# Optimization experiments

Hardware: AMD Instinct MI355X
Metric: run time of the kernel (lower is better)

Reference implementation:

```python
import jax, jax.numpy as jnp
import numpy as np

B, L, D = 2, 2048, 512
H = 8
DH = D // H
MAX_DIST = 2048
DFC = 2048


def setup_inputs() -> dict:
    key = jax.random.key(0)
    ks = jax.random.split(key, 12)
    w = lambda k, shape: (jax.random.normal(k, shape, jnp.float32) * 0.02)
    x = jax.random.normal(ks[0], (B, L, D), jnp.float32)
    # additive causal mask: 0 on/below diagonal, -1e9 above
    mask = jnp.where(jnp.triu(jnp.ones((L, L), bool), 1), -1e9, 0.0).astype(jnp.float32)
    return {
        "x": x,
        "mask": mask,
        "wq": w(ks[1], (D, D)), "bq": jnp.zeros((D,), jnp.float32),
        "wk": w(ks[2], (D, D)), "bk": jnp.zeros((D,), jnp.float32),
        "wv": w(ks[3], (D, D)), "bv": jnp.zeros((D,), jnp.float32),
        "rel_emb": w(ks[4], (MAX_DIST, D)),
        "w1": w(ks[5], (D, DFC)), "b1": jnp.zeros((DFC,), jnp.float32),
        "w2": w(ks[6], (DFC, D)), "b2": jnp.zeros((D,), jnp.float32),
    }


def skew(q_e):
    # Huang et al. sec 3.4: pad one column on the left, reshape (L, L+1)->(L+1, L), drop first row
    b, h, l, _ = q_e.shape
    padded = jnp.pad(q_e, ((0, 0), (0, 0), (0, 0), (1, 0)))  # (B,H,L,L+1)
    return padded.reshape(b, h, l + 1, l)[:, :, 1:, :]        # (B,H,L,L)


def reference(x, mask, wq, bq, wk, bk, wv, bv, rel_emb, w1, b1, w2, b2):
    b, l, d = x.shape
    q = (x @ wq + bq).reshape(b, l, H, DH)
    k = (x @ wk + bk).reshape(b, l, H, DH)
    v = (x @ wv + bv).reshape(b, l, H, DH)
    # relative position embeddings for the last l positions
    e = rel_emb[rel_emb.shape[0] - l:].reshape(l, H, DH)       # (L,H,DH)
    q_e = jnp.einsum('blhd,mhd->bhlm', q, e)                   # QE^T
    s_rel = skew(q_e)
    qk = jnp.einsum('blhd,bmhd->bhlm', q, k)                   # QK^T
    logits = (qk + s_rel) / jnp.sqrt(jnp.float32(DH)) + mask
    a = jax.nn.softmax(logits, axis=-1)
    attn = jnp.einsum('bhlm,bmhd->blhd', a, v).reshape(b, l, d)
    h = jax.nn.relu(attn @ w1 + b1)  # dropout is identity in eval mode
    return h @ w2 + b2
```

## Files before the change

### kernel.cpp

```cpp
#include <hip/hip_runtime.h>
#include <cstdint>

#define B_   2
#define L_   2048
#define D_   512
#define H_   8
#define DH_  64
#define DFC_ 2048

typedef unsigned short ushort_t;
typedef __attribute__((ext_vector_type(8))) short bf16x8;
typedef __attribute__((ext_vector_type(4))) short bf16x4;
typedef __attribute__((ext_vector_type(4))) float f32x4;

#define MFMA32(A, Bv, C) __builtin_amdgcn_mfma_f32_16x16x32_bf16(A, Bv, C, 0, 0, 0)
#define MFMA16(A, Bv, C) __builtin_amdgcn_mfma_f32_16x16x16bf16_1k(A, Bv, C, 0, 0, 0)

__device__ __forceinline__ ushort_t f32_bf16(float f) {
  unsigned u = __float_as_uint(f);
  u += 0x7FFFu + ((u >> 16) & 1u);
  return (ushort_t)(u >> 16);
}
__device__ __forceinline__ float bf16_f32(ushort_t u) {
  return __uint_as_float(((unsigned)u) << 16);
}

__device__ __forceinline__ void gl_lds16(const ushort_t* g, ushort_t* l) {
  __builtin_amdgcn_global_load_lds(
      (const __attribute__((address_space(1))) void*)(const void*)g,
      (__attribute__((address_space(3))) void*)l, 16, 0, 0);
}

__global__ __launch_bounds__(256)
void pack_x_rel(const float* __restrict__ x, const float* __restrict__ rel,
                ushort_t* __restrict__ xb, ushort_t* __restrict__ relb) {
  const int bid = blockIdx.x;
  const float* in = (bid < 1024) ? x : rel;
  ushort_t* out = (bid < 1024) ? xb : relb;
  const int base = (bid < 1024) ? bid : (bid - 1024);
  int i = (base * 256 + threadIdx.x) * 8;
  float4 a = *(const float4*)(in + i);
  float4 b = *(const float4*)(in + i + 4);
  union { bf16x8 v; ushort_t s[8]; } u;
  u.s[0] = f32_bf16(a.x); u.s[1] = f32_bf16(a.y);
  u.s[2] = f32_bf16(a.z); u.s[3] = f32_bf16(a.w);
  u.s[4] = f32_bf16(b.x); u.s[5] = f32_bf16(b.y);
  u.s[6] = f32_bf16(b.z); u.s[7] = f32_bf16(b.w);
  *(bf16x8*)(out + i) = u.v;
}

__global__ __launch_bounds__(256)
void packT_all(const float* __restrict__ wq, const float* __restrict__ wk,
               const float* __restrict__ wv, const float* __restrict__ w1,
               const float* __restrict__ w2, ushort_t* __restrict__ wqkvT,
               ushort_t* __restrict__ w1T, ushort_t* __restrict__ w2T) {
  __shared__ float T[64 * 65];
  const int id = blockIdx.x;
  const float* in; ushort_t* out; int K, N, bx, by;
  if (id < 192) {
    int z = id >> 6, r = id & 63;
    in = (z == 0) ? wq : (z == 1) ? wk : wv;
    out = wqkvT + (size_t)z * 512 * 512;
    K = 512; N = 512; bx = r & 7; by = r >> 3;
  } else if (id < 448) {
    int r = id - 192;
    in = w1; out = w1T; K = 512; N = 2048; bx = r & 31; by = r >> 5;
  } else {
    int r = id - 448;
    in = w2; out = w2T; K = 2048; N = 512; bx = r & 7; by = r >> 3;
  }
  const int t = threadIdx.x;
  const int n0 = bx * 64, k0 = by * 64;
  {
    const int kr = t >> 2, c0 = (t & 3) * 16;
    const float* src = in + (size_t)(k0 + kr) * N + n0 + c0;
#pragma unroll
    for (int u = 0; u < 4; ++u) {
      float4 f = *(const float4*)(src + u * 4);
      T[kr * 65 + c0 + u * 4 + 0] = f.x;
      T[kr * 65 + c0 + u * 4 + 1] = f.y;
      T[kr * 65 + c0 + u * 4 + 2] = f.z;
      T[kr * 65 + c0 + u * 4 + 3] = f.w;
    }
  }
  __syncthreads();
  const int nr = t >> 2, kc0 = (t & 3) * 16;
  union { bf16x8 v; ushort_t s[8]; } o0, o1;
#pragma unroll
  for (int j = 0; j < 8; ++j) {
    o0.s[j] = f32_bf16(T[(kc0 + j) * 65 + nr]);
    o1.s[j] = f32_bf16(T[(kc0 + 8 + j) * 65 + nr]);
  }
  ushort_t* dst = out + (size_t)(n0 + nr) * K + k0 + kc0;
  *(bf16x8*)dst = o0.v;
  *(bf16x8*)(dst + 8) = o1.v;
}

template <int MODE>
__global__ __launch_bounds__(256, 2)
void gemm_mfma(const ushort_t* __restrict__ A, const ushort_t* __restrict__ Bt,
               const float* __restrict__ b0p, const float* __restrict__ b1p,
               const float* __restrict__ b2p,
               void* __restrict__ out0, void* __restrict__ out1, void* __restrict__ out2,
               int M, int N, int K, int ksplit) {
  __shared__ ushort_t As[128 * 32];
  __shared__ ushort_t Bs[128 * 32];

  const int t  = threadIdx.x;
  const int wv = t >> 6, ln = t & 63;
  const int l16 = ln & 15, lg = ln >> 4;
  const int n0 = blockIdx.x * 128, m0 = blockIdx.y * 128;
  const int mw = (wv >> 1) * 64, nw = (wv & 1) * 64;

  const int kchunk = K / ksplit;
  const int kbeg = blockIdx.z * kchunk, kend = kbeg + kchunk;

  f32x4 acc[4][4] = {};

  for (int k0 = kbeg; k0 < kend; k0 += 32) {
    __syncthreads();
#pragma unroll
    for (int i = 0; i < 2; ++i) {
      const int s = (i * 4 + wv) * 64 + ln;
      const int row = s >> 2, cs = s & 3;
      const int g = cs ^ ((row >> 1) & 3);
      gl_lds16(A + (size_t)(m0 + row) * K + k0 + g * 8, &As[(i * 4 + wv) * 512]);
      gl_lds16(Bt + (size_t)(n0 + row) * K + k0 + g * 8, &Bs[(i * 4 + wv) * 512]);
    }
    __syncthreads();

    bf16x8 af[4], bfr[4];
#pragma unroll
    for (int mi = 0; mi < 4; ++mi) {
      const int ri = mw + mi * 16 + l16;
      af[mi] = *(const bf16x8*)&As[ri * 32 + ((lg ^ ((ri >> 1) & 3)) * 8)];
    }
#pragma unroll
    for (int ni = 0; ni < 4; ++ni) {
      const int rj = nw + ni * 16 + l16;
      bfr[ni] = *(const bf16x8*)&Bs[rj * 32 + ((lg ^ ((rj >> 1) & 3)) * 8)];
    }
#pragma unroll
    for (int mi = 0; mi < 4; ++mi)
#pragma unroll
      for (int ni = 0; ni < 4; ++ni)
        acc[mi][ni] = MFMA32(af[mi], bfr[ni], acc[mi][ni]);
  }

  if (MODE == 0) {
    float* outp = (blockIdx.z == 0) ? (float*)out0 : (float*)out1;
#pragma unroll
    for (int mi = 0; mi < 4; ++mi)
#pragma unroll
      for (int reg = 0; reg < 4; ++reg) {
        const int m = m0 + mw + mi * 16 + lg * 4 + reg;
#pragma unroll
        for (int ni = 0; ni < 4; ++ni) {
          const int c = n0 + nw + ni * 16 + l16;
          outp[(size_t)m * N + c] = acc[mi][ni][reg];
        }
      }
  } else if (MODE == 1) {
    ushort_t* outp = (ushort_t*)out0;
#pragma unroll
    for (int mi = 0; mi < 4; ++mi)
#pragma unroll
      for (int reg = 0; reg < 4; ++reg) {
        const int m = m0 + mw + mi * 16 + lg * 4 + reg;
#pragma unroll
        for (int ni = 0; ni < 4; ++ni) {
          const int c = n0 + nw + ni * 16 + l16;
          float v = acc[mi][ni][reg] + b0p[c];
          outp[(size_t)m * N + c] = f32_bf16(fmaxf(v, 0.f));
        }
      }
  } else {
#pragma unroll
    for (int mi = 0; mi < 4; ++mi)
#pragma unroll
      for (int reg = 0; reg < 4; ++reg) {
        const int m = m0 + mw + mi * 16 + lg * 4 + reg;
        const int b = m >> 11, l = m & (L_ - 1);
#pragma unroll
        for (int ni = 0; ni < 4; ++ni) {
          const int c = n0 + nw + ni * 16 + l16;
          const int which = c >> 9, cc = c & 511;
          const int h = cc >> 6, dh = cc & 63;
          const float* bias = (which == 0) ? b0p : (which == 1) ? b1p : b2p;
          float v = acc[mi][ni][reg] + bias[cc];
          if (which == 0) {
            ((ushort_t*)out0)[(((size_t)b * H_ + h) * L_ + l) * DH_ + dh] =
                f32_bf16(v * 0.125f);
          } else if (which == 1) {
            ((ushort_t*)out1)[(((size_t)b * H_ + h) * L_ + l) * DH_ + dh] = f32_bf16(v);
          } else {
            ((ushort_t*)out2)[(((size_t)b * H_ + h) * DH_ + dh) * L_ + l] = f32_bf16(v);
          }
        }
      }
  }
}

__global__ __launch_bounds__(256)
void ffn2_add(float* __restrict__ out, const float* __restrict__ p1,
              const float* __restrict__ bias) {
  int i = (blockIdx.x * 256 + threadIdx.x) * 4;
  float4 a = *(const float4*)(out + i);
  float4 b = *(const float4*)(p1 + i);
  float4 bb = *(const float4*)(bias + (i & (D_ - 1)));
  a.x += b.x + bb.x; a.y += b.y + bb.y;
  a.z += b.z + bb.z; a.w += b.w + bb.w;
  *(float4*)(out + i) = a;
}

__global__ __launch_bounds__(256, 4)
void attn_mfma(const ushort_t* __restrict__ q16, const ushort_t* __restrict__ k16,
               const ushort_t* __restrict__ vT, const ushort_t* __restrict__ relb,
               float* __restrict__ Opart, float* __restrict__ Lpart) {
  __shared__ ushort_t Ks[64 * 64];
  __shared__ ushort_t Vs[64 * 64];
  __shared__ ushort_t Rc[64 * 136];

  const int t   = threadIdx.x;
  const int wv  = t >> 6;
  const int ln  = t & 63;
  const int l16 = ln & 15;
  const int lg  = ln >> 4;
  const int bh  = blockIdx.x;
  const int yy  = blockIdx.y;
  const int qb  = (yy < 16) ? yy : (47 - yy);
  const int z   = blockIdx.z;
  const int i0  = qb * 64;
  const int mid = (qb + 2) >> 1;
  const int kbeg = z ? mid : 0;
  const int kend = z ? (qb + 1) : mid;

  const ushort_t* qh = q16 + (size_t)bh * L_ * DH_;
  const ushort_t* kh = k16 + (size_t)bh * L_ * DH_;
  const ushort_t* vh = vT + (size_t)bh * DH_ * L_;
  const ushort_t* relh = relb + (bh & 7) * DH_;

  const int r64i = wv * 16 + l16;
  const int rrow = r64i * 136;

  bf16x8 qf0, qf1;
  {
    const ushort_t* qr = qh + (size_t)(i0 + r64i) * DH_ + lg * 8;
    qf0 = *(const bf16x8*)(qr);
    qf1 = *(const bf16x8*)(qr + 32);
  }

  const f32x4 zf = {0.f, 0.f, 0.f, 0.f};
  f32x4 Of[4] = {zf, zf, zf, zf};
  float lsum = 0.f;

  auto compute_R = [&](int mbase, int slotbase) {
#pragma unroll
    for (int cb = 0; cb < 4; ++cb) {
      const ushort_t* e = relh + (size_t)(mbase + cb * 16 + l16) * D_ + lg * 8;
      bf16x8 e0 = *(const bf16x8*)(e);
      bf16x8 e1 = *(const bf16x8*)(e + 32);
      f32x4 r = MFMA32(e0, qf0, zf);
      r = MFMA32(e1, qf1, r);
      ushort4 w;
      w.x = f32_bf16(r[0]); w.y = f32_bf16(r[1]);
      w.z = f32_bf16(r[2]); w.w = f32_bf16(r[3]);
      *(ushort4*)&Rc[rrow + slotbase + cb * 16 + lg * 4] = w;
      if (slotbase == 0 && cb == 0 && lg == 0)
        *(ushort4*)&Rc[rrow + 128] = w;
    }
  };

  if (kbeg < kend) {
    compute_R(L_ - 64 - i0 + kbeg * 64, (kbeg & 1) * 64);

    for (int kb = kbeg; kb < kend; ++kb) {
      const int j0 = kb * 64;
      __syncthreads();
#pragma unroll
      for (int i = 0; i < 2; ++i) {
        const int s = (i * 4 + wv) * 64 + ln;
        const int row = s >> 3, c = s & 7;
        const int g = c ^ (row & 7);
        gl_lds16(kh + (size_t)(j0 + row) * DH_ + g * 8, &Ks[(i * 4 + wv) * 512]);
        gl_lds16(vh + (size_t)row * L_ + j0 + g * 8, &Vs[(i * 4 + wv) * 512]);
      }
      if (kb < qb)
        compute_R(L_ - 64 - i0 + (kb + 1) * 64, ((kb + 1) & 1) * 64);
      __syncthreads();

      f32x4 sf[4];
#pragma unroll
      for (int cb = 0; cb < 4; ++cb) {
        const int j = cb * 16 + l16;
        const int sw = j & 7;
        bf16x8 k0 = *(const bf16x8*)&Ks[j * 64 + ((lg ^ sw) * 8)];
        bf16x8 k1 = *(const bf16x8*)&Ks[j * 64 + (((lg + 4) ^ sw) * 8)];
        f32x4 s = MFMA32(k0, qf0, zf);
        sf[cb] = MFMA32(k1, qf1, s);
      }

      const bool diag = (kb == qb);
      bf16x4 pa[4];
#pragma unroll
      for (int cb = 0; cb < 4; ++cb) {
        const int jj0 = cb * 16 + lg * 4;
        const int base = (j0 + jj0 + 63 - r64i) & 127;
        union { bf16x4 v; ushort_t s[4]; } pk;
#pragma unroll
        for (int reg = 0; reg < 4; ++reg) {
          float x = sf[cb][reg] + bf16_f32(Rc[rrow + base + reg]);
          if (diag && (jj0 + reg) > r64i) x = -1e30f;
          float p = __expf(x);
          lsum += p;
          pk.s[reg] = f32_bf16(p);
        }
        pa[cb] = pk.v;
      }

#pragma unroll
      for (int cb2 = 0; cb2 < 4; ++cb2) {
        const int dh = cb2 * 16 + l16;
        const int sw = dh & 7;
        const ushort_t* vrow = &Vs[dh * 64];
#pragma unroll
        for (int cb = 0; cb < 4; ++cb) {
          const int cc = cb * 2 + (lg >> 1);
          bf16x4 vf = *(const bf16x4*)&vrow[((cc ^ sw) * 8) + (lg & 1) * 4];
          Of[cb2] = MFMA16(vf, pa[cb], Of[cb2]);
        }
      }
    }
  }

  float tot = lsum;
  tot += __shfl_xor(tot, 16);
  tot += __shfl_xor(tot, 32);
  if (lg == 0)
    Lpart[((size_t)(z * 16 + bh)) * L_ + i0 + r64i] = tot;
  float* orow = Opart + (((size_t)(z * 16 + bh)) * L_ + i0 + r64i) * DH_;
#pragma unroll
  for (int cb2 = 0; cb2 < 4; ++cb2)
    *(f32x4*)&orow[cb2 * 16 + lg * 4] = Of[cb2];
}

__global__ __launch_bounds__(256)
void attn_combine(const float* __restrict__ Opart, const float* __restrict__ Lpart,
                  ushort_t* __restrict__ attnb) {
  const int g = blockIdx.x * 256 + threadIdx.x;
  const int dh4 = g & 15, i = (g >> 4) & (L_ - 1), bh = g >> 15;
  const size_t o0 = (((size_t)bh * L_ + i) * DH_) + dh4 * 4;
  const size_t zstride = (size_t)16 * L_ * DH_;
  float4 a = *(const float4*)(Opart + o0);
  float4 b = *(const float4*)(Opart + o0 + zstride);
  const float l = Lpart[(size_t)bh * L_ + i] + Lpart[(size_t)(16 + bh) * L_ + i];
  const float inv = 1.f / l;
  ushort4 o;
  o.x = f32_bf16((a.x + b.x) * inv);
  o.y = f32_bf16((a.y + b.y) * inv);
  o.z = f32_bf16((a.z + b.z) * inv);
  o.w = f32_bf16((a.w + b.w) * inv);
  const int bb = bh >> 3, h = bh & 7;
  *(ushort4*)(attnb + ((size_t)(bb * L_ + i)) * D_ + h * DH_ + dh4 * 4) = o;
}

extern "C" void kernel_launch(void* const* d_in, const int* in_sizes, int n_in,
                              void* d_out, int out_size, void* d_ws, size_t ws_size,
                              hipStream_t stream) {
  const float* x   = (const float*)d_in[0];
  const float* wq  = (const float*)d_in[2];
  const float* bq  = (const float*)d_in[3];
  const float* wk  = (const float*)d_in[4];
  const float* bk  = (const float*)d_in[5];
  const float* wv  = (const float*)d_in[6];
  const float* bv  = (const float*)d_in[7];
  const float* rel = (const float*)d_in[8];
  const float* w1  = (const float*)d_in[9];
  const float* b1  = (const float*)d_in[10];
  const float* w2  = (const float*)d_in[11];
  const float* b2  = (const float*)d_in[12];

  char* wsb = (char*)d_ws;
  const size_t MB = 1u << 20;
  ushort_t* xb     = (ushort_t*)(wsb + 0 * MB);
  ushort_t* attnb  = (ushort_t*)(wsb + 0 * MB);
  ushort_t* wqkvT  = (ushort_t*)(wsb + 4 * MB);
  ushort_t* w1T    = (ushort_t*)(wsb + 6 * MB);
  ushort_t* w2T    = (ushort_t*)(wsb + 8 * MB);
  ushort_t* relb   = (ushort_t*)(wsb + 10 * MB);
  ushort_t* q16    = (ushort_t*)(wsb + 12 * MB);
  ushort_t* k16    = (ushort_t*)(wsb + 16 * MB);
  ushort_t* vTb    = (ushort_t*)(wsb + 20 * MB);
  float*    Opart  = (float*)(wsb + 24 * MB);
  float*    Lpart  = (float*)(wsb + 40 * MB);
  ushort_t* hidb   = (ushort_t*)(wsb + 24 * MB);
  float*    p1     = (float*)(wsb + 12 * MB);
  float*    out    = (float*)d_out;

  dim3 blk(256);
  pack_x_rel<<<dim3(1536), blk, 0, stream>>>(x, rel, xb, relb);
  packT_all<<<dim3(704), blk, 0, stream>>>(wq, wk, wv, w1, w2, wqkvT, w1T, w2T);
  gemm_mfma<2><<<dim3(12, 32), blk, 0, stream>>>(
      xb, wqkvT, bq, bk, bv, q16, k16, vTb, B_ * L_, 1536, D_, 1);
  attn_mfma<<<dim3(16, 32, 2), blk, 0, stream>>>(q16, k16, vTb, relb, Opart, Lpart);
  attn_combine<<<dim3(2048), blk, 0, stream>>>(Opart, Lpart, attnb);
  gemm_mfma<1><<<dim3(16, 32), blk, 0, stream>>>(
      attnb, w1T, b1, nullptr, nullptr, hidb, nullptr, nullptr,
      B_ * L_, DFC_, D_, 1);
  gemm_mfma<0><<<dim3(4, 32, 2), blk, 0, stream>>>(
      hidb, w2T, nullptr, nullptr, nullptr, out, p1, nullptr,
      B_ * L_, D_, DFC_, 2);
  ffn2_add<<<dim3(2048), blk, 0, stream>>>(out, p1, b2);
}
```

Baseline: 232.9 us.

## Double-buffer LDS tiles in GEMM and attention, merge packing kernels

The GEMM and attention kernels now keep two LDS buffers for their A/B and K/V tiles. The next tile's global-to-LDS load is issued before computing on the current tile, and each loop iteration drops one barrier. This is meant to hide global load latency behind MFMA work. The cost is doubled LDS use, and the attention kernel's launch bound is lowered from 4 to 3 blocks per CU to fit it. The two input/weight packing kernels are also merged into one launch to save launch overhead.

```diff
diff --git a/kernel.cpp b/kernel.cpp
--- a/kernel.cpp
+++ b/kernel.cpp
@@ -32,30 +32,32 @@
 }
 
 __global__ __launch_bounds__(256)
-void pack_x_rel(const float* __restrict__ x, const float* __restrict__ rel,
-                ushort_t* __restrict__ xb, ushort_t* __restrict__ relb) {
+void pack_all(const float* __restrict__ x, const float* __restrict__ rel,
+              const float* __restrict__ wq, const float* __restrict__ wk,
+              const float* __restrict__ wv, const float* __restrict__ w1,
+              const float* __restrict__ w2,
+              ushort_t* __restrict__ xb, ushort_t* __restrict__ relb,
+              ushort_t* __restrict__ wqkvT, ushort_t* __restrict__ w1T,
+              ushort_t* __restrict__ w2T) {
+  __shared__ float T[64 * 65];
   const int bid = blockIdx.x;
-  const float* in = (bid < 1024) ? x : rel;
-  ushort_t* out = (bid < 1024) ? xb : relb;
-  const int base = (bid < 1024) ? bid : (bid - 1024);
-  int i = (base * 256 + threadIdx.x) * 8;
-  float4 a = *(const float4*)(in + i);
-  float4 b = *(const float4*)(in + i + 4);
-  union { bf16x8 v; ushort_t s[8]; } u;
-  u.s[0] = f32_bf16(a.x); u.s[1] = f32_bf16(a.y);
-  u.s[2] = f32_bf16(a.z); u.s[3] = f32_bf16(a.w);
-  u.s[4] = f32_bf16(b.x); u.s[5] = f32_bf16(b.y);
-  u.s[6] = f32_bf16(b.z); u.s[7] = f32_bf16(b.w);
-  *(bf16x8*)(out + i) = u.v;
-}
-
-__global__ __launch_bounds__(256)
-void packT_all(const float* __restrict__ wq, const float* __restrict__ wk,
-               const float* __restrict__ wv, const float* __restrict__ w1,
-               const float* __restrict__ w2, ushort_t* __restrict__ wqkvT,
-               ushort_t* __restrict__ w1T, ushort_t* __restrict__ w2T) {
-  __shared__ float T[64 * 65];
-  const int id = blockIdx.x;
+  const int t = threadIdx.x;
+  if (bid < 1536) {
+    const float* in = (bid < 1024) ? x : rel;
+    ushort_t* out = (bid < 1024) ? xb : relb;
+    const int base = (bid < 1024) ? bid : (bid - 1024);
+    int i = (base * 256 + t) * 8;
+    float4 a = *(const float4*)(in + i);
+    float4 b = *(const float4*)(in + i + 4);
+    union { bf16x8 v; ushort_t s[8]; } u;
+    u.s[0] = f32_bf16(a.x); u.s[1] = f32_bf16(a.y);
+    u.s[2] = f32_bf16(a.z); u.s[3] = f32_bf16(a.w);
+    u.s[4] = f32_bf16(b.x); u.s[5] = f32_bf16(b.y);
+    u.s[6] = f32_bf16(b.z); u.s[7] = f32_bf16(b.w);
+    *(bf16x8*)(out + i) = u.v;
+    return;
+  }
+  const int id = bid - 1536;
   const float* in; ushort_t* out; int K, N, bx, by;
   if (id < 192) {
     int z = id >> 6, r = id & 63;
@@ -69,7 +71,6 @@
     int r = id - 448;
     in = w2; out = w2T; K = 2048; N = 512; bx = r & 7; by = r >> 3;
   }
-  const int t = threadIdx.x;
   const int n0 = bx * 64, k0 = by * 64;
   {
     const int kr = t >> 2, c0 = (t & 3) * 16;
@@ -103,8 +104,8 @@
                const float* __restrict__ b2p,
                void* __restrict__ out0, void* __restrict__ out1, void* __restrict__ out2,
                int M, int N, int K, int ksplit) {
-  __shared__ ushort_t As[128 * 32];
-  __shared__ ushort_t Bs[128 * 32];
+  __shared__ ushort_t As[2][128 * 32];
+  __shared__ ushort_t Bs[2][128 * 32];
 
   const int t  = threadIdx.x;
   const int wv = t >> 6, ln = t & 63;
@@ -117,34 +118,40 @@
 
   f32x4 acc[4][4] = {};
 
-  for (int k0 = kbeg; k0 < kend; k0 += 32) {
-    __syncthreads();
+  auto stage = [&](int k0, int b) {
 #pragma unroll
     for (int i = 0; i < 2; ++i) {
       const int s = (i * 4 + wv) * 64 + ln;
       const int row = s >> 2, cs = s & 3;
       const int g = cs ^ ((row >> 1) & 3);
-      gl_lds16(A + (size_t)(m0 + row) * K + k0 + g * 8, &As[(i * 4 + wv) * 512]);
-      gl_lds16(Bt + (size_t)(n0 + row) * K + k0 + g * 8, &Bs[(i * 4 + wv) * 512]);
-    }
+      gl_lds16(A + (size_t)(m0 + row) * K + k0 + g * 8, &As[b][(i * 4 + wv) * 512]);
+      gl_lds16(Bt + (size_t)(n0 + row) * K + k0 + g * 8, &Bs[b][(i * 4 + wv) * 512]);
+    }
+  };
+
+  stage(kbeg, 0);
+  int buf = 0;
+  for (int k0 = kbeg; k0 < kend; k0 += 32) {
     __syncthreads();
+    if (k0 + 32 < kend) stage(k0 + 32, buf ^ 1);
 
     bf16x8 af[4], bfr[4];
 #pragma unroll
     for (int mi = 0; mi < 4; ++mi) {
       const int ri = mw + mi * 16 + l16;
-      af[mi] = *(const bf16x8*)&As[ri * 32 + ((lg ^ ((ri >> 1) & 3)) * 8)];
+      af[mi] = *(const bf16x8*)&As[buf][ri * 32 + ((lg ^ ((ri >> 1) & 3)) * 8)];
     }
 #pragma unroll
     for (int ni = 0; ni < 4; ++ni) {
       const int rj = nw + ni * 16 + l16;
-      bfr[ni] = *(const bf16x8*)&Bs[rj * 32 + ((lg ^ ((rj >> 1) & 3)) * 8)];
+      bfr[ni] = *(const bf16x8*)&Bs[buf][rj * 32 + ((lg ^ ((rj >> 1) & 3)) * 8)];
     }
 #pragma unroll
     for (int mi = 0; mi < 4; ++mi)
 #pragma unroll
       for (int ni = 0; ni < 4; ++ni)
         acc[mi][ni] = MFMA32(af[mi], bfr[ni], acc[mi][ni]);
+    buf ^= 1;
   }
 
   if (MODE == 0) {
@@ -213,12 +220,12 @@
   *(float4*)(out + i) = a;
 }
 
-__global__ __launch_bounds__(256, 4)
+__global__ __launch_bounds__(256, 3)
 void attn_mfma(const ushort_t* __restrict__ q16, const ushort_t* __restrict__ k16,
                const ushort_t* __restrict__ vT, const ushort_t* __restrict__ relb,
                float* __restrict__ Opart, float* __restrict__ Lpart) {
-  __shared__ ushort_t Ks[64 * 64];
-  __shared__ ushort_t Vs[64 * 64];
+  __shared__ ushort_t Ks[2][64 * 64];
+  __shared__ ushort_t Vs[2][64 * 64];
   __shared__ ushort_t Rc[64 * 136];
 
   const int t   = threadIdx.x;
@@ -254,6 +261,17 @@
   f32x4 Of[4] = {zf, zf, zf, zf};
   float lsum = 0.f;
 
+  auto stageKV = [&](int j0, int b) {
+#pragma unroll
+    for (int i = 0; i < 2; ++i) {
+      const int s = (i * 4 + wv) * 64 + ln;
+      const int row = s >> 3, c = s & 7;
+      const int g = c ^ (row & 7);
+      gl_lds16(kh + (size_t)(j0 + row) * DH_ + g * 8, &Ks[b][(i * 4 + wv) * 512]);
+      gl_lds16(vh + (size_t)row * L_ + j0 + g * 8, &Vs[b][(i * 4 + wv) * 512]);
+    }
+  };
+
   auto compute_R = [&](int mbase, int slotbase) {
 #pragma unroll
     for (int cb = 0; cb < 4; ++cb) {
@@ -272,30 +290,24 @@
   };
 
   if (kbeg < kend) {
+    stageKV(kbeg * 64, kbeg & 1);
     compute_R(L_ - 64 - i0 + kbeg * 64, (kbeg & 1) * 64);
 
     for (int kb = kbeg; kb < kend; ++kb) {
       const int j0 = kb * 64;
+      const int buf = kb & 1;
       __syncthreads();
-#pragma unroll
-      for (int i = 0; i < 2; ++i) {
-        const int s = (i * 4 + wv) * 64 + ln;
-        const int row = s >> 3, c = s & 7;
-        const int g = c ^ (row & 7);
-        gl_lds16(kh + (size_t)(j0 + row) * DH_ + g * 8, &Ks[(i * 4 + wv) * 512]);
-        gl_lds16(vh + (size_t)row * L_ + j0 + g * 8, &Vs[(i * 4 + wv) * 512]);
-      }
+      if (kb + 1 < kend) stageKV(j0 + 64, buf ^ 1);
       if (kb < qb)
         compute_R(L_ - 64 - i0 + (kb + 1) * 64, ((kb + 1) & 1) * 64);
-      __syncthreads();
 
       f32x4 sf[4];
 #pragma unroll
       for (int cb = 0; cb < 4; ++cb) {
         const int j = cb * 16 + l16;
         const int sw = j & 7;
-        bf16x8 k0 = *(const bf16x8*)&Ks[j * 64 + ((lg ^ sw) * 8)];
-        bf16x8 k1 = *(const bf16x8*)&Ks[j * 64 + (((lg + 4) ^ sw) * 8)];
+        bf16x8 k0 = *(const bf16x8*)&Ks[buf][j * 64 + ((lg ^ sw) * 8)];
+        bf16x8 k1 = *(const bf16x8*)&Ks[buf][j * 64 + (((lg + 4) ^ sw) * 8)];
         f32x4 s = MFMA32(k0, qf0, zf);
         sf[cb] = MFMA32(k1, qf1, s);
       }
@@ -322,7 +334,7 @@
       for (int cb2 = 0; cb2 < 4; ++cb2) {
         const int dh = cb2 * 16 + l16;
         const int sw = dh & 7;
-        const ushort_t* vrow = &Vs[dh * 64];
+        const ushort_t* vrow = &Vs[buf][dh * 64];
 #pragma unroll
         for (int cb = 0; cb < 4; ++cb) {
           const int cc = cb * 2 + (lg >> 1);
@@ -398,8 +410,8 @@
   float*    out    = (float*)d_out;
 
   dim3 blk(256);
-  pack_x_rel<<<dim3(1536), blk, 0, stream>>>(x, rel, xb, relb);
-  packT_all<<<dim3(704), blk, 0, stream>>>(wq, wk, wv, w1, w2, wqkvT, w1T, w2T);
+  pack_all<<<dim3(2240), blk, 0, stream>>>(x, rel, wq, wk, wv, w1, w2,
+                                           xb, relb, wqkvT, w1T, w2T);
   gemm_mfma<2><<<dim3(12, 32), blk, 0, stream>>>(
       xb, wqkvT, bq, bk, bv, q16, k16, vTb, B_ * L_, 1536, D_, 1);
   attn_mfma<<<dim3(16, 32, 2), blk, 0, stream>>>(q16, k16, vTb, relb, Opart, Lpart);
```

After: 243.7 us. +4.7%, slower.
